# Performance work log

Measured on AMD Instinct MI355X. Metric: run time of the kernel, lower is better.

Reference implementation:

```python
import jax, jax.numpy as jnp
import numpy as np

HIDDEN_DIM = 4096
MM_DIM = 7


def setup_inputs() -> dict:
    key = jax.random.key(0)
    k_img, k_a = jax.random.split(key)
    images = jax.random.normal(k_img, (64, 576, MM_DIM), dtype=jnp.float32)
    # Fixed orthogonal buffer A, as in load_model: QR of a random gaussian matrix.
    rm = np.asarray(jax.random.normal(k_a, (HIDDEN_DIM, HIDDEN_DIM), dtype=jnp.float32))
    Q, _ = np.linalg.qr(rm.astype(np.float64), mode='complete')
    A = jnp.asarray(Q.astype(np.float32))
    return {"images": images, "A": A}


def reference(images, A):
    # Original: F.pad(x, (0, hidden_dim - mm_dim)) @ A.
    # Zero-padded columns contribute nothing, so this is exactly
    # x @ A[:mm_dim, :]  (a [*, 7] x [7, 4096] contraction).
    return jnp.einsum('btm,mh->bth', images, A[:MM_DIM, :])
```

## Files before the change

### kernel.cpp

```cpp
#include <hip/hip_runtime.h>


typedef float f4 __attribute__((ext_vector_type(4)));

#define NROWS  (64 * 576)
#define HID    4096
#define MM     7
#define NW     4
#define BLOCKS 2048
#define RPB    18
#define SUB    6

__global__ __launch_bounds__(256, 3) void vt_kernel(const float* __restrict__ images,
                                                    const float* __restrict__ A,
                                                    float* __restrict__ out) {
    const int tid  = threadIdx.x;
    const int row0 = blockIdx.x * RPB;

    f4 a[NW][MM];
#pragma unroll
    for (int it = 0; it < NW; ++it) {
#pragma unroll
        for (int m = 0; m < MM; ++m) {
            a[it][m] = *(const f4*)(A + (size_t)m * HID + (it << 10) + (tid << 2));
        }
    }

    for (int g = 0; g < RPB / SUB; ++g) {
        const int r0 = row0 + g * SUB;

        float x[SUB][MM];
#pragma unroll
        for (int r = 0; r < SUB; ++r) {
#pragma unroll
            for (int m = 0; m < MM; ++m) {
                x[r][m] = images[(size_t)(r0 + r) * MM + m];
            }
        }

#pragma unroll
        for (int r = 0; r < SUB; ++r) {
            float* orow = out + (size_t)(r0 + r) * HID + (tid << 2);
#pragma unroll
            for (int it = 0; it < NW; ++it) {
                f4 acc = x[r][0] * a[it][0];
#pragma unroll
                for (int m = 1; m < MM; ++m) {
                    acc += x[r][m] * a[it][m];
                }
                *(f4*)(orow + (it << 10)) = acc;
            }
        }
    }
}

extern "C" void kernel_launch(void* const* d_in, const int* in_sizes, int n_in,
                              void* d_out, int out_size, void* d_ws, size_t ws_size,
                              hipStream_t stream) {
    const float* images = (const float*)d_in[0];
    const float* A      = (const float*)d_in[1];
    float* out          = (float*)d_out;

    vt_kernel<<<BLOCKS, 256, 0, stream>>>(images, A, out);
}
```

Measured before the change: 622.7 us.

## Split columns across block pairs, prefetch inputs, use nontemporal stores

Each row-slot is now split across two blocks, each covering half of the hidden columns. This halves the per-thread A register footprint and raises the occupancy target to 4. The next group of image rows is prefetched while the current group is computed, and the row values are made wave-uniform via readfirstlane. Output stores become nontemporal to avoid polluting cache on the write-only output stream. The trade-off is twice as many blocks and doubled reads of the image rows.

```diff
diff --git a/kernel.cpp b/kernel.cpp
--- a/kernel.cpp
+++ b/kernel.cpp
@@ -6,50 +6,62 @@
 #define NROWS  (64 * 576)
 #define HID    4096
 #define MM     7
-#define NW     4
-#define BLOCKS 2048
 #define RPB    18
 #define SUB    6
+#define NG     (RPB / SUB)
+#define SLOTS  (NROWS / RPB)
+#define BLOCKS (SLOTS * 2)
 
-__global__ __launch_bounds__(256, 3) void vt_kernel(const float* __restrict__ images,
+__global__ __launch_bounds__(256, 4) void vt_kernel(const float* __restrict__ images,
                                                     const float* __restrict__ A,
                                                     float* __restrict__ out) {
     const int tid  = threadIdx.x;
-    const int row0 = blockIdx.x * RPB;
+    const int slot = (int)blockIdx.x >> 1;
+    const int half = (int)blockIdx.x & 1;
+    const int row0 = slot * RPB;
+    const int c0   = (half << 11) + (tid << 2);
 
-    f4 a[NW][MM];
+    f4 a0[MM], a1[MM];
 #pragma unroll
-    for (int it = 0; it < NW; ++it) {
-#pragma unroll
-        for (int m = 0; m < MM; ++m) {
-            a[it][m] = *(const f4*)(A + (size_t)m * HID + (it << 10) + (tid << 2));
-        }
+    for (int m = 0; m < MM; ++m) {
+        a0[m] = *(const f4*)(A + (size_t)m * HID + c0);
+        a1[m] = *(const f4*)(A + (size_t)m * HID + c0 + 1024);
     }
 
-    for (int g = 0; g < RPB / SUB; ++g) {
-        const int r0 = row0 + g * SUB;
+    float xv[SUB * MM];
+    {
+        const float* ip = images + (size_t)row0 * MM;
+#pragma unroll
+        for (int i = 0; i < SUB * MM; ++i) xv[i] = ip[i];
+    }
 
-        float x[SUB][MM];
+#pragma unroll
+    for (int g = 0; g < NG; ++g) {
+        float xs[SUB * MM];
+#pragma unroll
+        for (int i = 0; i < SUB * MM; ++i)
+            xs[i] = __int_as_float(__builtin_amdgcn_readfirstlane(__float_as_int(xv[i])));
+
+        if (g + 1 < NG) {
+            const float* ip = images + (size_t)(row0 + (g + 1) * SUB) * MM;
+#pragma unroll
+            for (int i = 0; i < SUB * MM; ++i) xv[i] = ip[i];
+        }
+
+        float* orow = out + (size_t)(row0 + g * SUB) * HID + c0;
 #pragma unroll
         for (int r = 0; r < SUB; ++r) {
+            const int xb = r * MM;
+            f4 acc0 = xs[xb] * a0[0];
+            f4 acc1 = xs[xb] * a1[0];
 #pragma unroll
-            for (int m = 0; m < MM; ++m) {
-                x[r][m] = images[(size_t)(r0 + r) * MM + m];
+            for (int m = 1; m < MM; ++m) {
+                acc0 += xs[xb + m] * a0[m];
+                acc1 += xs[xb + m] * a1[m];
             }
-        }
-
-#pragma unroll
-        for (int r = 0; r < SUB; ++r) {
-            float* orow = out + (size_t)(r0 + r) * HID + (tid << 2);
-#pragma unroll
-            for (int it = 0; it < NW; ++it) {
-                f4 acc = x[r][0] * a[it][0];
-#pragma unroll
-                for (int m = 1; m < MM; ++m) {
-                    acc += x[r][m] * a[it][m];
-                }
-                *(f4*)(orow + (it << 10)) = acc;
-            }
+            __builtin_nontemporal_store(acc0, (f4*)orow);
+            __builtin_nontemporal_store(acc1, (f4*)(orow + 1024));
+            orow += HID;
         }
     }
 }
```

New measurement: 625.2 us. Within noise of the previous version (+0.4%).
